# Performance work log

Hardware: AMD Instinct MI355X
Metric: run time of the kernel (lower is better)

The kernel has to match this reference:

```python
import jax, jax.numpy as jnp
import numpy as np

D_MODEL = 1024
N_HEADS = 16
D_HEAD = D_MODEL // N_HEADS
B = 2
Q_LEN = 1024
MEM_LEN = 1024
K_LEN = MEM_LEN + Q_LEN


def _split_heads(x, n_heads):
    b, t, d = x.shape
    return x.reshape(b, t, n_heads, d // n_heads).transpose(0, 2, 1, 3)


def _rel_shift(x):
    # x: [b, h, q, k] -> Transformer-XL relative shift
    b, h, q_len, k_len = x.shape
    x = jnp.pad(x, ((0, 0), (0, 0), (0, 0), (1, 0)))
    x = x.reshape(b, h, k_len + 1, q_len)
    x = x[:, :, 1:, :]
    return x.reshape(b, h, q_len, k_len)


def setup_inputs() -> dict:
    key = jax.random.key(0)
    ks = jax.random.split(key, 10)
    s = 1.0 / np.sqrt(D_MODEL)  # lecun_normal-ish scale for kernels
    return {
        "h": jax.random.normal(ks[0], (B, Q_LEN, D_MODEL), jnp.float32),
        "mem": jax.random.normal(ks[1], (B, MEM_LEN, D_MODEL), jnp.float32),
        "r": jax.random.normal(ks[2], (K_LEN, D_MODEL), jnp.float32),
        "Wq": jax.random.normal(ks[3], (D_MODEL, D_MODEL), jnp.float32) * s,
        "Wk": jax.random.normal(ks[4], (D_MODEL, D_MODEL), jnp.float32) * s,
        "Wv": jax.random.normal(ks[5], (D_MODEL, D_MODEL), jnp.float32) * s,
        "Wr": jax.random.normal(ks[6], (D_MODEL, D_MODEL), jnp.float32) * s,
        "Wo": jax.random.normal(ks[7], (D_MODEL, D_MODEL), jnp.float32) * s,
        "r_w_bias": jnp.zeros((N_HEADS, D_HEAD), jnp.float32),
        "r_r_bias": jnp.zeros((N_HEADS, D_HEAD), jnp.float32),
    }


def reference(h, mem, r, Wq, Wk, Wv, Wr, Wo, r_w_bias, r_r_bias):
    k_len = mem.shape[1] + h.shape[1]
    cat = jnp.concatenate([mem, h], axis=1)           # [b, k, d]
    q = _split_heads(h @ Wq, N_HEADS)                  # [b, h, q, dh]
    k = _split_heads(cat @ Wk, N_HEADS)                # [b, h, k, dh]
    v = _split_heads(cat @ Wv, N_HEADS)                # [b, h, k, dh]
    r_head = (r @ Wr).reshape(k_len, N_HEADS, D_HEAD).transpose(1, 0, 2)  # [h, k, dh]

    qw = q + r_w_bias[None, :, None, :]
    ac = jnp.einsum('bhqd,bhkd->bhqk', qw, k)          # content score
    qr = q + r_r_bias[None, :, None, :]
    bd = _rel_shift(jnp.einsum('bhqd,hkd->bhqk', qr, r_head))  # position score

    attn_score = (ac + bd) / jnp.sqrt(jnp.array(D_HEAD, jnp.float32))
    attn_prob = jax.nn.softmax(attn_score, axis=-1)
    attn_vec = jnp.einsum('bhqk,bhkd->bhqd', attn_prob, v)
    b, nh, t, dh = attn_vec.shape
    attn_vec = attn_vec.transpose(0, 2, 1, 3).reshape(b, t, nh * dh)
    return attn_vec @ Wo
```

## Files before the change

kernel.cpp:

```cpp
#include <hip/hip_runtime.h>

#define DM 1024
#define NH 16
#define DH 64
#define QL 1024
#define KL 2048

typedef short s16x8 __attribute__((ext_vector_type(8)));
typedef float f32x4 __attribute__((ext_vector_type(4)));

__device__ __forceinline__ unsigned short f2bf(float f) {
  unsigned int u = __builtin_bit_cast(unsigned int, f);
  u += 0x7fffu + ((u >> 16) & 1u);
  return (unsigned short)(u >> 16);
}
__device__ __forceinline__ float bf2f(unsigned short b) {
  unsigned int u = ((unsigned int)b) << 16;
  return __builtin_bit_cast(float, u);
}
__device__ __forceinline__ f32x4 mfma16(s16x8 a, s16x8 b, f32x4 c) {
  return __builtin_amdgcn_mfma_f32_16x16x32_bf16(a, b, c, 0, 0, 0);
}
__device__ __forceinline__ void gl2lds16(const void* g, void* l) {
  __builtin_amdgcn_global_load_lds(
      (const __attribute__((address_space(1))) unsigned int*)g,
      (__attribute__((address_space(3))) unsigned int*)l, 16, 0, 0);
}


__global__ __launch_bounds__(256) void prep_all(
    const float* __restrict__ h, const float* __restrict__ mem, const float* __restrict__ r,
    const float* __restrict__ Wq, const float* __restrict__ Wk, const float* __restrict__ Wv,
    const float* __restrict__ Wr, const float* __restrict__ Wo,
    unsigned short* __restrict__ catb, unsigned short* __restrict__ rb,
    unsigned short* __restrict__ wqt, unsigned short* __restrict__ wkvt,
    unsigned short* __restrict__ wrt,
    unsigned short* __restrict__ wohi, unsigned short* __restrict__ wolo)
{
  __shared__ unsigned short tH[64][72];
  __shared__ unsigned short tL[64][72];
  if (blockIdx.x < 6144) {
    int idx = blockIdx.x * 256 + threadIdx.x;
    if (idx < 1048576) {
      int e = idx * 4;
      int row = e >> 10, col = e & 1023;
      int b = row >> 11, t = row & 2047;
      const float* s = (t < 1024) ? &mem[((size_t)(b * 1024 + t)) * 1024 + col]
                                  : &h[((size_t)(b * 1024 + t - 1024)) * 1024 + col];
      float4 v = *(const float4*)s;
      *(ushort4*)&catb[e] = make_ushort4(f2bf(v.x), f2bf(v.y), f2bf(v.z), f2bf(v.w));
    } else {
      int e = (idx - 1048576) * 4;
      float4 v = *(const float4*)&r[e];
      *(ushort4*)&rb[e] = make_ushort4(f2bf(v.x), f2bf(v.y), f2bf(v.z), f2bf(v.w));
    }
    return;
  }
  int q = blockIdx.x - 6144;
  int job = q >> 8;
  int tb = q & 255;
  int sr0 = (tb >> 4) * 64, sc0 = (tb & 15) * 64;
  const float* src = (job == 0) ? Wq : (job == 1) ? Wk : (job == 2) ? Wv : (job == 3) ? Wr : Wo;
  int tid = threadIdx.x;
  int rr = tid >> 4, c4 = (tid & 15) * 4;
#pragma unroll
  for (int i = 0; i < 4; ++i) {
    int row = rr + i * 16;
    float4 v = *(const float4*)&src[(size_t)(sr0 + row) * 1024 + sc0 + c4];
    float vv[4] = {v.x, v.y, v.z, v.w};
#pragma unroll
    for (int j = 0; j < 4; ++j) {
      unsigned short hi = f2bf(vv[j]);
      tH[c4 + j][row] = hi;
      if (job == 4) tL[c4 + j][row] = f2bf(vv[j] - bf2f(hi));
    }
  }
  __syncthreads();
  unsigned short* dst = (job == 0) ? wqt : (job == 1) ? wkvt
                      : (job == 2) ? (wkvt + (size_t)1024 * 1024)
                      : (job == 3) ? wrt : wohi;
#pragma unroll
  for (int i = 0; i < 4; ++i) {
    int row = rr + i * 16;
    size_t o = (size_t)(sc0 + row) * 1024 + sr0 + c4;
    *(ushort4*)&dst[o] = make_ushort4(tH[row][c4], tH[row][c4 + 1], tH[row][c4 + 2], tH[row][c4 + 3]);
    if (job == 4)
      *(ushort4*)&wolo[o] = make_ushort4(tL[row][c4], tL[row][c4 + 1], tL[row][c4 + 2], tL[row][c4 + 3]);
  }
}

__global__ __launch_bounds__(256) void gemm_all(
    const unsigned short* __restrict__ catb, const unsigned short* __restrict__ rb,
    const unsigned short* __restrict__ wqt, const unsigned short* __restrict__ wkvt,
    const unsigned short* __restrict__ wrt,
    const float* __restrict__ rwb, const float* __restrict__ rrb,
    unsigned short* __restrict__ qwP, unsigned short* __restrict__ qrP,
    unsigned short* __restrict__ kP, unsigned short* __restrict__ vP,
    unsigned short* __restrict__ rP)
{
  __shared__ __align__(16) unsigned short As[2 * 128 * 32];
  __shared__ __align__(16) unsigned short Bs[2 * 128 * 32];
  int blk = blockIdx.x, tid = threadIdx.x;
  int job, mb, nb;
  const unsigned short *A, *Bt;
  if (blk < 128)      { job = 0; A = catb; Bt = wqt;  mb = blk >> 3; nb = blk & 7; }
  else if (blk < 640) { job = 1; A = catb; Bt = wkvt; int q = blk - 128; mb = q >> 4; nb = q & 15; }
  else                { job = 2; A = rb;   Bt = wrt;  int q = blk - 640; mb = q >> 3; nb = q & 7; }

  const int w = tid >> 6;
  const int r0 = tid >> 2;
  const int c0u = (tid & 3) * 8;
  int ga_r0 = mb * 128 + r0, ga_r1 = mb * 128 + 64 + r0;
  if (job == 0) {
    ga_r0 = ((ga_r0 >> 10) << 11) + 1024 + (ga_r0 & 1023);
    ga_r1 = ((ga_r1 >> 10) << 11) + 1024 + (ga_r1 & 1023);
  }
  const unsigned short* gA0 = A + (size_t)ga_r0 * 1024 + c0u;
  const unsigned short* gA1 = A + (size_t)ga_r1 * 1024 + c0u;
  const unsigned short* gB0 = Bt + (size_t)(nb * 128 + r0) * 1024 + c0u;
  const unsigned short* gB1 = Bt + (size_t)(nb * 128 + 64 + r0) * 1024 + c0u;
  char* lA0 = (char*)As + w * 1024;  char* lA1 = (char*)As + 4096 + w * 1024;
  char* lB0 = (char*)Bs + w * 1024;  char* lB1 = (char*)Bs + 4096 + w * 1024;

  const int lane = tid & 63;
  const int lc = lane & 15, quad = lane >> 4;
  const int wm = (w & 1) * 64, wn = (w >> 1) * 64;

  f32x4 acc[4][4];
#pragma unroll
  for (int mt = 0; mt < 4; ++mt)
#pragma unroll
    for (int nt = 0; nt < 4; ++nt) { acc[mt][nt][0] = 0.f; acc[mt][nt][1] = 0.f; acc[mt][nt][2] = 0.f; acc[mt][nt][3] = 0.f; }

  for (int k0 = 0; k0 < 1024; k0 += 64) {
    __syncthreads();
    gl2lds16(gA0 + k0, lA0);
    gl2lds16(gA1 + k0, lA1);
    gl2lds16(gB0 + k0, lB0);
    gl2lds16(gB1 + k0, lB1);
    gl2lds16(gA0 + k0 + 32, lA0 + 8192);
    gl2lds16(gA1 + k0 + 32, lA1 + 8192);
    gl2lds16(gB0 + k0 + 32, lB0 + 8192);
    gl2lds16(gB1 + k0 + 32, lB1 + 8192);
    __syncthreads();
#pragma unroll
    for (int s = 0; s < 2; ++s) {
      s16x8 af[4], bfr[4];
#pragma unroll
      for (int mt = 0; mt < 4; ++mt) af[mt] = *(const s16x8*)&As[s * 4096 + (wm + mt * 16 + lc) * 32 + quad * 8];
#pragma unroll
      for (int nt = 0; nt < 4; ++nt) bfr[nt] = *(const s16x8*)&Bs[s * 4096 + (wn + nt * 16 + lc) * 32 + quad * 8];
#pragma unroll
      for (int mt = 0; mt < 4; ++mt)
#pragma unroll
        for (int nt = 0; nt < 4; ++nt) acc[mt][nt] = mfma16(af[mt], bfr[nt], acc[mt][nt]);
    }
  }

#pragma unroll
  for (int mt = 0; mt < 4; ++mt) {
    int t4 = mb * 128 + wm + mt * 16 + quad * 4;
#pragma unroll
    for (int nt = 0; nt < 4; ++nt) {
      int n = nb * 128 + wn + nt * 16 + lc;
      if (job == 0) {
        int hh = n >> 6, dh = n & 63;
        int f = dh >> 5, qd = (dh >> 3) & 3, j = dh & 7;
        float bw = rwb[n], br = rrb[n];
        int bb = t4 >> 10, trow = t4 & 1023;
        size_t tbb = ((((size_t)(bb * NH + hh) * 64 + (trow >> 4)) * 2 + f) * 512) + qd * 128 + j;
        int l0 = trow & 15;
#pragma unroll
        for (int rr = 0; rr < 4; ++rr) {
          qwP[tbb + (l0 + rr) * 8] = f2bf(acc[mt][nt][rr] + bw);
          qrP[tbb + (l0 + rr) * 8] = f2bf(acc[mt][nt][rr] + br);
        }
      } else if (job == 1) {
        int bb = t4 >> 11, t = t4 & 2047;
        if (n < 1024) {
          int hh = n >> 6, dh = n & 63;
          int f = dh >> 5, qd = (dh >> 3) & 3, j = dh & 7;
          size_t tbb = ((((size_t)(bb * NH + hh) * 128 + (t >> 4)) * 2 + f) * 512) + qd * 128 + j;
          int l0 = t & 15;
#pragma unroll
          for (int rr = 0; rr < 4; ++rr)
            kP[tbb + (l0 + rr) * 8] = f2bf(acc[mt][nt][rr]);
        } else {
          int n2 = n - 1024, hh = n2 >> 6, dh = n2 & 63;
          int bhv = bb * NH + hh;
          int kt = t >> 5;
          int ntv = dh >> 4;
          int lanev = (((t >> 3) & 3) << 4) + (dh & 15);
          ushort4 pk = make_ushort4(f2bf(acc[mt][nt][0]), f2bf(acc[mt][nt][1]),
                                    f2bf(acc[mt][nt][2]), f2bf(acc[mt][nt][3]));
          *(ushort4*)&vP[(((size_t)bhv * 64 + kt) * 4 + ntv) * 512 + lanev * 8 + (t & 7)] = pk;
        }
      } else {
        int hh = n >> 6, dh = n & 63;
        int f = dh >> 5, qd = (dh >> 3) & 3, j = dh & 7;
        size_t tbb = (((size_t)hh * 128 + (t4 >> 4)) * 2 + f) * 512 + qd * 128 + j;
        int l0 = t4 & 15;
#pragma unroll
        for (int rr = 0; rr < 4; ++rr)
          rP[tbb + (l0 + rr) * 8] = f2bf(acc[mt][nt][rr]);
      }
    }
  }
}

#define BDSTR 2058
__global__ __launch_bounds__(512, 4) void attn(
    const unsigned short* __restrict__ qwP, const unsigned short* __restrict__ qrP,
    const unsigned short* __restrict__ kP, const unsigned short* __restrict__ vP,
    const unsigned short* __restrict__ rP,
    unsigned short* __restrict__ avhi, unsigned short* __restrict__ avlo)
{
  __shared__ __align__(16) unsigned short bdS[17 * BDSTR];
  __shared__ __align__(16) unsigned short pS[8 * 16 * 36];
  float* oS = (float*)bdS;
  float* lS = (float*)bdS + 8192;

  const int tid = threadIdx.x;
  const int w = tid >> 6, lane = tid & 63;
  const int lc = lane & 15, quad = lane >> 4;
  const int is = blockIdx.x & 63, h = (blockIdx.x >> 6) & 15, b = blockIdx.x >> 10;
  const int i0 = is * 16;
  const size_t bh = (size_t)b * NH + h;

  const unsigned short* qwP_p = qwP + bh * 65536;
  const unsigned short* qrP_p = qrP + bh * 65536;
  const unsigned short* kP_p  = kP + bh * 131072;
  const unsigned short* vP_p  = vP + bh * (size_t)KL * DH + lane * 8;
  const unsigned short* rP_p  = rP + (size_t)h * 131072;

  {
    const int cmax = 1006 - i0;
    s16x8 qa00 = *(const s16x8*)(qrP_p + is * 1024 + lane * 8);
    s16x8 qa01 = *(const s16x8*)(qrP_p + is * 1024 + 512 + lane * 8);
    int r1 = i0 + 16 + lc; if (r1 > 1023) r1 = 1023;
    int off1 = (r1 >> 4) * 1024 + (quad * 16 + (r1 & 15)) * 8;
    s16x8 qa10 = *(const s16x8*)(qrP_p + off1);
    s16x8 qa11 = *(const s16x8*)(qrP_p + off1 + 512);
    const int xt0 = w * 16;
    const unsigned short* rp = rP_p + xt0 * 1024 + lane * 8;
    s16x8 rf0 = *(const s16x8*)rp;
    s16x8 rf1 = *(const s16x8*)(rp + 512);
    for (int xt = xt0; xt < xt0 + 16; ++xt) {
      s16x8 cf0 = rf0, cf1 = rf1;
      if (xt + 1 < xt0 + 16) {
        const unsigned short* rpn = rP_p + (xt + 1) * 1024 + lane * 8;
        rf0 = *(const s16x8*)rpn;
        rf1 = *(const s16x8*)(rpn + 512);
      }
      f32x4 c0; c0[0] = 0.f; c0[1] = 0.f; c0[2] = 0.f; c0[3] = 0.f;
      c0 = mfma16(qa00, cf0, c0); c0 = mfma16(qa01, cf1, c0);
      int col = xt * 16 + lc;
#pragma unroll
      for (int rr = 0; rr < 4; ++rr) bdS[(quad * 4 + rr) * BDSTR + col] = f2bf(c0[rr]);
      if (xt * 16 <= cmax) {
        f32x4 c1; c1[0] = 0.f; c1[1] = 0.f; c1[2] = 0.f; c1[3] = 0.f;
        c1 = mfma16(qa10, cf0, c1); c1 = mfma16(qa11, cf1, c1);
        if (lane < 16) bdS[16 * BDSTR + col] = f2bf(c1[0]);
      }
    }
  }
  __syncthreads();

  s16x8 qwf0 = *(const s16x8*)(qwP_p + is * 1024 + lane * 8);
  s16x8 qwf1 = *(const s16x8*)(qwP_p + is * 1024 + 512 + lane * 8);

  f32x4 O[4];
#pragma unroll
  for (int nt = 0; nt < 4; ++nt) { O[nt][0] = 0.f; O[nt][1] = 0.f; O[nt][2] = 0.f; O[nt][3] = 0.f; }
  float lsum[4] = {0.f, 0.f, 0.f, 0.f};
  unsigned short* pw = pS + w * 16 * 36;
  int ebase[4];
#pragma unroll
  for (int rr = 0; rr < 4; ++rr) ebase[rr] = lc - (quad * 4 + rr) - i0;

  auto gatherBD = [&](int k0, float bd[2][4]) {
#pragma unroll
    for (int tt = 0; tt < 2; ++tt)
#pragma unroll
      for (int rr = 0; rr < 4; ++rr) {
        int row = quad * 4 + rr;
        int d = k0 + tt * 16 + ebase[rr];
        int am = row * BDSTR + (d + 1023);
        int aw = (row + 1) * BDSTR + (d - 1026);
        unsigned short vb = bdS[(d <= 1024) ? am : aw];
        bd[tt][rr] = (d == 1025) ? 0.0f : bf2f(vb);
      }
  };
  auto loadK4 = [&](int k0, s16x8& a0, s16x8& a1, s16x8& b0, s16x8& b1) {
    const unsigned short* kp = kP_p + (size_t)(k0 >> 4) * 1024 + lane * 8;
    a0 = *(const s16x8*)kp;
    a1 = *(const s16x8*)(kp + 512);
    b0 = *(const s16x8*)(kp + 1024);
    b1 = *(const s16x8*)(kp + 1536);
  };
  const float E2S = 0.18033688011112042f;
  const float E2B = -17.312340490667562f;
  auto qkExp = [&](const s16x8& a0, const s16x8& a1, const s16x8& b0, const s16x8& b1,
                   const float bd[2][4], float p[2][4]) {
    f32x4 c;
    c[0] = bd[0][0]; c[1] = bd[0][1]; c[2] = bd[0][2]; c[3] = bd[0][3];
    c = mfma16(qwf0, a0, c);
    c = mfma16(qwf1, a1, c);
#pragma unroll
    for (int rr = 0; rr < 4; ++rr) {
      p[0][rr] = __builtin_amdgcn_exp2f(fmaf(c[rr], E2S, E2B));
      lsum[rr] += p[0][rr];
    }
    f32x4 d;
    d[0] = bd[1][0]; d[1] = bd[1][1]; d[2] = bd[1][2]; d[3] = bd[1][3];
    d = mfma16(qwf0, b0, d);
    d = mfma16(qwf1, b1, d);
#pragma unroll
    for (int rr = 0; rr < 4; ++rr) {
      p[1][rr] = __builtin_amdgcn_exp2f(fmaf(d[rr], E2S, E2B));
      lsum[rr] += p[1][rr];
    }
  };
  auto storeP = [&](float p[2][4]) {
#pragma unroll
    for (int rr = 0; rr < 4; ++rr) {
      int row = quad * 4 + rr;
      pw[row * 36 + lc]      = f2bf(p[0][rr]);
      pw[row * 36 + 16 + lc] = f2bf(p[1][rr]);
    }
  };
  auto loadV = [&](int k0, s16x8 vf[4]) {
    const unsigned short* base = vP_p + (size_t)(k0 >> 5) * 2048;
#pragma unroll
    for (int nt = 0; nt < 4; ++nt)
      vf[nt] = *(const s16x8*)(base + nt * 512);
  };

  s16x8 ka0, ka1, kb0, kb1;
  s16x8 vfPrev[4];
  loadK4(w * 256, ka0, ka1, kb0, kb1);
  loadV(w * 256, vfPrev);
  {
    float bd[2][4], p[2][4];
    gatherBD(w * 256, bd);
    s16x8 na0, na1, nb0, nb1;
    loadK4(w * 256 + 32, na0, na1, nb0, nb1);
    qkExp(ka0, ka1, kb0, kb1, bd, p);
    storeP(p);
    ka0 = na0; ka1 = na1; kb0 = nb0; kb1 = nb1;
  }
#pragma unroll 1
  for (int it = 1; it < 8; ++it) {
    const int k0 = w * 256 + it * 32;
    __builtin_amdgcn_s_waitcnt(0xC07F);
    s16x8 pf = *(const s16x8*)(pw + lc * 36 + quad * 8);
    float bd[2][4], p[2][4];
    gatherBD(k0, bd);
    s16x8 na0, na1, nb0, nb1;
    const int kn = k0 + ((it < 7) ? 32 : 0);
    loadK4(kn, na0, na1, nb0, nb1);
#pragma unroll
    for (int nt = 0; nt < 4; ++nt) O[nt] = mfma16(pf, vfPrev[nt], O[nt]);
    loadV(k0, vfPrev);
    qkExp(ka0, ka1, kb0, kb1, bd, p);
    storeP(p);
    ka0 = na0; ka1 = na1; kb0 = nb0; kb1 = nb1;
  }
  {
    __builtin_amdgcn_s_waitcnt(0xC07F);
    s16x8 pf = *(const s16x8*)(pw + lc * 36 + quad * 8);
#pragma unroll
    for (int nt = 0; nt < 4; ++nt) O[nt] = mfma16(pf, vfPrev[nt], O[nt]);
  }

#pragma unroll
  for (int msk = 1; msk <= 8; msk <<= 1)
#pragma unroll
    for (int rr = 0; rr < 4; ++rr) lsum[rr] += __shfl_xor(lsum[rr], msk);

  __syncthreads();
#pragma unroll
  for (int nt = 0; nt < 4; ++nt)
#pragma unroll
    for (int rr = 0; rr < 4; ++rr)
      oS[(w * 16 + quad * 4 + rr) * 64 + nt * 16 + lc] = O[nt][rr];
  if (lc == 0) {
#pragma unroll
    for (int rr = 0; rr < 4; ++rr) lS[w * 16 + quad * 4 + rr] = lsum[rr];
  }
  __syncthreads();

  if (tid < 256) {
    int r = tid >> 4, c0 = (tid & 15) * 4;
    float L = 0.f, a0 = 0.f, a1 = 0.f, a2 = 0.f, a3 = 0.f;
#pragma unroll
    for (int wv = 0; wv < 8; ++wv) {
      L += lS[wv * 16 + r];
      const float* op = oS + (wv * 16 + r) * 64 + c0;
      a0 += op[0]; a1 += op[1]; a2 += op[2]; a3 += op[3];
    }
    float inv = 1.0f / L;
    float v[4] = {a0 * inv, a1 * inv, a2 * inv, a3 * inv};
    unsigned short hi[4], lo[4];
#pragma unroll
    for (int j = 0; j < 4; ++j) {
      hi[j] = f2bf(v[j]);
      lo[j] = f2bf(v[j] - bf2f(hi[j]));
    }
    size_t oidx = ((size_t)(b * QL + i0 + r)) * DM + h * DH + c0;
    *(ushort4*)&avhi[oidx] = make_ushort4(hi[0], hi[1], hi[2], hi[3]);
    *(ushort4*)&avlo[oidx] = make_ushort4(lo[0], lo[1], lo[2], lo[3]);
  }
}

__global__ __launch_bounds__(256) void gemm_final(
    const unsigned short* __restrict__ avhi, const unsigned short* __restrict__ avlo,
    const unsigned short* __restrict__ wohi, const unsigned short* __restrict__ wolo,
    float* __restrict__ out)
{
  __shared__ __align__(16) unsigned short S[4][2][64 * 32];
  int blk = blockIdx.x, tid = threadIdx.x;
  int mb = blk >> 4, nb = blk & 15;

  const int w = tid >> 6, lane = tid & 63;
  const int srow = w * 16 + (lane >> 2);
  const int scu = (lane & 3) * 8;
  const size_t arow = (size_t)(mb * 64 + srow) * 1024 + scu;
  const size_t brow = (size_t)(nb * 64 + srow) * 1024 + scu;
  char* l0 = (char*)&S[0][0][0] + w * 1024;
  char* l1 = (char*)&S[1][0][0] + w * 1024;
  char* l2 = (char*)&S[2][0][0] + w * 1024;
  char* l3 = (char*)&S[3][0][0] + w * 1024;

  const int lc = lane & 15, quad = lane >> 4;
  const int wm = (w & 1) * 32, wn = (w >> 1) * 32;

  f32x4 acc[2][2];
#pragma unroll
  for (int mt = 0; mt < 2; ++mt)
#pragma unroll
    for (int nt = 0; nt < 2; ++nt) { acc[mt][nt][0] = 0.f; acc[mt][nt][1] = 0.f; acc[mt][nt][2] = 0.f; acc[mt][nt][3] = 0.f; }

  for (int k0 = 0; k0 < 1024; k0 += 64) {
    __syncthreads();
    gl2lds16(avhi + arow + k0, l0);
    gl2lds16(avhi + arow + k0 + 32, l0 + 4096);
    gl2lds16(avlo + arow + k0, l1);
    gl2lds16(avlo + arow + k0 + 32, l1 + 4096);
    gl2lds16(wohi + brow + k0, l2);
    gl2lds16(wohi + brow + k0 + 32, l2 + 4096);
    gl2lds16(wolo + brow + k0, l3);
    gl2lds16(wolo + brow + k0 + 32, l3 + 4096);
    __syncthreads();
#pragma unroll
    for (int s = 0; s < 2; ++s) {
      s16x8 ah[2], al[2], bh[2], bl[2];
#pragma unroll
      for (int mt = 0; mt < 2; ++mt) {
        int off = (wm + mt * 16 + lc) * 32 + quad * 8;
        ah[mt] = *(const s16x8*)&S[0][s][off];
        al[mt] = *(const s16x8*)&S[1][s][off];
      }
#pragma unroll
      for (int nt = 0; nt < 2; ++nt) {
        int off = (wn + nt * 16 + lc) * 32 + quad * 8;
        bh[nt] = *(const s16x8*)&S[2][s][off];
        bl[nt] = *(const s16x8*)&S[3][s][off];
      }
#pragma unroll
      for (int mt = 0; mt < 2; ++mt)
#pragma unroll
        for (int nt = 0; nt < 2; ++nt) {
          acc[mt][nt] = mfma16(ah[mt], bh[nt], acc[mt][nt]);
          acc[mt][nt] = mfma16(ah[mt], bl[nt], acc[mt][nt]);
          acc[mt][nt] = mfma16(al[mt], bh[nt], acc[mt][nt]);
        }
    }
  }

#pragma unroll
  for (int mt = 0; mt < 2; ++mt)
#pragma unroll
    for (int nt = 0; nt < 2; ++nt) {
      int n = nb * 64 + wn + nt * 16 + lc;
#pragma unroll
      for (int rr = 0; rr < 4; ++rr) {
        int m = mb * 64 + wm + mt * 16 + quad * 4 + rr;
        out[(size_t)m * 1024 + n] = acc[mt][nt][rr];
      }
    }
}

extern "C" void kernel_launch(void* const* d_in, const int* in_sizes, int n_in,
                              void* d_out, int out_size, void* d_ws, size_t ws_size,
                              hipStream_t stream) {
  (void)in_sizes; (void)n_in; (void)out_size; (void)ws_size;
  const float* h   = (const float*)d_in[0];
  const float* mem = (const float*)d_in[1];
  const float* r   = (const float*)d_in[2];
  const float* Wq  = (const float*)d_in[3];
  const float* Wk  = (const float*)d_in[4];
  const float* Wv  = (const float*)d_in[5];
  const float* Wr  = (const float*)d_in[6];
  const float* Wo  = (const float*)d_in[7];
  const float* rwb = (const float*)d_in[8];
  const float* rrb = (const float*)d_in[9];
  float* out = (float*)d_out;

  char* ws = (char*)d_ws;
  unsigned short* catb = (unsigned short*)(ws + 0);
  unsigned short* rb   = (unsigned short*)(ws + 8388608);
  unsigned short* wqt  = (unsigned short*)(ws + 12582912);
  unsigned short* wkvt = (unsigned short*)(ws + 14680064);
  unsigned short* wrt  = (unsigned short*)(ws + 18874368);
  unsigned short* wohi = (unsigned short*)(ws + 20971520);
  unsigned short* wolo = (unsigned short*)(ws + 23068672);
  unsigned short* qwP  = (unsigned short*)(ws + 25165824);
  unsigned short* qrP  = (unsigned short*)(ws + 29360128);
  unsigned short* kPb  = (unsigned short*)(ws + 33554432);
  unsigned short* vPb  = (unsigned short*)(ws + 41943040);
  unsigned short* rPb  = (unsigned short*)(ws + 50331648);
  unsigned short* avhi = (unsigned short*)(ws + 54525952);
  unsigned short* avlo = (unsigned short*)(ws + 58720256);

  prep_all<<<7424, 256, 0, stream>>>(h, mem, r, Wq, Wk, Wv, Wr, Wo,
                                     catb, rb, wqt, wkvt, wrt, wohi, wolo);
  gemm_all<<<768, 256, 0, stream>>>(catb, rb, wqt, wkvt, wrt, rwb, rrb,
                                    qwP, qrP, kPb, vPb, rPb);
  attn<<<2048, 512, 0, stream>>>(qwP, qrP, kPb, vPb, rPb, avhi, avlo);
  gemm_final<<<512, 256, 0, stream>>>(avhi, avlo, wohi, wolo, out);
}
```

Measured before the change: 260.3 us.

## Double-buffer GEMM k-tiles and pipeline attention BD gather and P·V

Both projection GEMMs (gemm_all and gemm_final) now use two LDS buffers with 32-wide k-steps. The next k-tile's global-to-LDS load is issued before the current tile's MFMAs, so memory latency overlaps compute. The attention inner loop now prefetches the next tile's rel-shift BD gather alongside the next K loads, and moves the P·V MFMA after the QK exponent work. It also drops the explicit s_waitcnt and instead reads the P fragment right after storing it. These changes trade extra registers (nbd, a second pf) for overlap, at some risk of lower occupancy or of relying on the compiler's LDS ordering.

```diff
diff --git a/kernel.cpp b/kernel.cpp
--- a/kernel.cpp
+++ b/kernel.cpp
@@ -98,8 +98,8 @@
     unsigned short* __restrict__ kP, unsigned short* __restrict__ vP,
     unsigned short* __restrict__ rP)
 {
-  __shared__ __align__(16) unsigned short As[2 * 128 * 32];
-  __shared__ __align__(16) unsigned short Bs[2 * 128 * 32];
+  __shared__ __align__(16) unsigned short As[2][128 * 32];
+  __shared__ __align__(16) unsigned short Bs[2][128 * 32];
   int blk = blockIdx.x, tid = threadIdx.x;
   int job, mb, nb;
   const unsigned short *A, *Bt;
@@ -119,42 +119,39 @@
   const unsigned short* gA1 = A + (size_t)ga_r1 * 1024 + c0u;
   const unsigned short* gB0 = Bt + (size_t)(nb * 128 + r0) * 1024 + c0u;
   const unsigned short* gB1 = Bt + (size_t)(nb * 128 + 64 + r0) * 1024 + c0u;
-  char* lA0 = (char*)As + w * 1024;  char* lA1 = (char*)As + 4096 + w * 1024;
-  char* lB0 = (char*)Bs + w * 1024;  char* lB1 = (char*)Bs + 4096 + w * 1024;
 
   const int lane = tid & 63;
   const int lc = lane & 15, quad = lane >> 4;
   const int wm = (w & 1) * 64, wn = (w >> 1) * 64;
 
+  auto stage = [&](int k0, int bi) {
+    gl2lds16(gA0 + k0, (char*)As[bi] + w * 1024);
+    gl2lds16(gA1 + k0, (char*)As[bi] + 4096 + w * 1024);
+    gl2lds16(gB0 + k0, (char*)Bs[bi] + w * 1024);
+    gl2lds16(gB1 + k0, (char*)Bs[bi] + 4096 + w * 1024);
+  };
+
   f32x4 acc[4][4];
 #pragma unroll
   for (int mt = 0; mt < 4; ++mt)
 #pragma unroll
     for (int nt = 0; nt < 4; ++nt) { acc[mt][nt][0] = 0.f; acc[mt][nt][1] = 0.f; acc[mt][nt][2] = 0.f; acc[mt][nt][3] = 0.f; }
 
-  for (int k0 = 0; k0 < 1024; k0 += 64) {
+  stage(0, 0);
+  __syncthreads();
+  for (int k0 = 0; k0 < 1024; k0 += 32) {
+    int cur = (k0 >> 5) & 1;
+    if (k0 + 32 < 1024) stage(k0 + 32, cur ^ 1);
+    s16x8 af[4], bfr[4];
+#pragma unroll
+    for (int mt = 0; mt < 4; ++mt) af[mt] = *(const s16x8*)&As[cur][(wm + mt * 16 + lc) * 32 + quad * 8];
+#pragma unroll
+    for (int nt = 0; nt < 4; ++nt) bfr[nt] = *(const s16x8*)&Bs[cur][(wn + nt * 16 + lc) * 32 + quad * 8];
+#pragma unroll
+    for (int mt = 0; mt < 4; ++mt)
+#pragma unroll
+      for (int nt = 0; nt < 4; ++nt) acc[mt][nt] = mfma16(af[mt], bfr[nt], acc[mt][nt]);
     __syncthreads();
-    gl2lds16(gA0 + k0, lA0);
-    gl2lds16(gA1 + k0, lA1);
-    gl2lds16(gB0 + k0, lB0);
-    gl2lds16(gB1 + k0, lB1);
-    gl2lds16(gA0 + k0 + 32, lA0 + 8192);
-    gl2lds16(gA1 + k0 + 32, lA1 + 8192);
-    gl2lds16(gB0 + k0 + 32, lB0 + 8192);
-    gl2lds16(gB1 + k0 + 32, lB1 + 8192);
-    __syncthreads();
-#pragma unroll
-    for (int s = 0; s < 2; ++s) {
-      s16x8 af[4], bfr[4];
-#pragma unroll
-      for (int mt = 0; mt < 4; ++mt) af[mt] = *(const s16x8*)&As[s * 4096 + (wm + mt * 16 + lc) * 32 + quad * 8];
-#pragma unroll
-      for (int nt = 0; nt < 4; ++nt) bfr[nt] = *(const s16x8*)&Bs[s * 4096 + (wn + nt * 16 + lc) * 32 + quad * 8];
-#pragma unroll
-      for (int mt = 0; mt < 4; ++mt)
-#pragma unroll
-        for (int nt = 0; nt < 4; ++nt) acc[mt][nt] = mfma16(af[mt], bfr[nt], acc[mt][nt]);
-    }
   }
 
 #pragma unroll
@@ -336,41 +333,52 @@
       vf[nt] = *(const s16x8*)(base + nt * 512);
   };
 
+  const int base = w * 256;
   s16x8 ka0, ka1, kb0, kb1;
-  s16x8 vfPrev[4];
-  loadK4(w * 256, ka0, ka1, kb0, kb1);
-  loadV(w * 256, vfPrev);
+  s16x8 vf[4];
+  s16x8 pf;
+  float bd[2][4], nbd[2][4];
+
+  gatherBD(base, bd);
+  loadK4(base, ka0, ka1, kb0, kb1);
+  loadV(base, vf);
   {
-    float bd[2][4], p[2][4];
-    gatherBD(w * 256, bd);
+    float p[2][4];
+    gatherBD(base + 32, nbd);
     s16x8 na0, na1, nb0, nb1;
-    loadK4(w * 256 + 32, na0, na1, nb0, nb1);
+    loadK4(base + 32, na0, na1, nb0, nb1);
     qkExp(ka0, ka1, kb0, kb1, bd, p);
     storeP(p);
+    pf = *(const s16x8*)(pw + lc * 36 + quad * 8);
     ka0 = na0; ka1 = na1; kb0 = nb0; kb1 = nb1;
+#pragma unroll
+    for (int tt = 0; tt < 2; ++tt)
+#pragma unroll
+      for (int rr = 0; rr < 4; ++rr) bd[tt][rr] = nbd[tt][rr];
   }
 #pragma unroll 1
-  for (int it = 1; it < 8; ++it) {
-    const int k0 = w * 256 + it * 32;
-    __builtin_amdgcn_s_waitcnt(0xC07F);
-    s16x8 pf = *(const s16x8*)(pw + lc * 36 + quad * 8);
-    float bd[2][4], p[2][4];
-    gatherBD(k0, bd);
+  for (int s = 1; s < 8; ++s) {
+    const int k0 = base + s * 32;
+    const int kn = base + ((s < 7) ? (s + 1) * 32 : s * 32);
+    float p[2][4];
+    gatherBD(kn, nbd);
     s16x8 na0, na1, nb0, nb1;
-    const int kn = k0 + ((it < 7) ? 32 : 0);
     loadK4(kn, na0, na1, nb0, nb1);
-#pragma unroll
-    for (int nt = 0; nt < 4; ++nt) O[nt] = mfma16(pf, vfPrev[nt], O[nt]);
-    loadV(k0, vfPrev);
     qkExp(ka0, ka1, kb0, kb1, bd, p);
+#pragma unroll
+    for (int nt = 0; nt < 4; ++nt) O[nt] = mfma16(pf, vf[nt], O[nt]);
+    loadV(k0, vf);
     storeP(p);
+    pf = *(const s16x8*)(pw + lc * 36 + quad * 8);
     ka0 = na0; ka1 = na1; kb0 = nb0; kb1 = nb1;
+#pragma unroll
+    for (int tt = 0; tt < 2; ++tt)
+#pragma unroll
+      for (int rr = 0; rr < 4; ++rr) bd[tt][rr] = nbd[tt][rr];
   }
   {
-    __builtin_amdgcn_s_waitcnt(0xC07F);
-    s16x8 pf = *(const s16x8*)(pw + lc * 36 + quad * 8);
-#pragma unroll
-    for (int nt = 0; nt < 4; ++nt) O[nt] = mfma16(pf, vfPrev[nt], O[nt]);
+#pragma unroll
+    for (int nt = 0; nt < 4; ++nt) O[nt] = mfma16(pf, vf[nt], O[nt]);
   }
 
 #pragma unroll
@@ -418,7 +426,7 @@
     const unsigned short* __restrict__ wohi, const unsigned short* __restrict__ wolo,
     float* __restrict__ out)
 {
-  __shared__ __align__(16) unsigned short S[4][2][64 * 32];
+  __shared__ __align__(16) unsigned short S[2][4][64 * 32];
   int blk = blockIdx.x, tid = threadIdx.x;
   int mb = blk >> 4, nb = blk & 15;
 
@@ -427,55 +435,50 @@
   const int scu = (lane & 3) * 8;
   const size_t arow = (size_t)(mb * 64 + srow) * 1024 + scu;
   const size_t brow = (size_t)(nb * 64 + srow) * 1024 + scu;
-  char* l0 = (char*)&S[0][0][0] + w * 1024;
-  char* l1 = (char*)&S[1][0][0] + w * 1024;
-  char* l2 = (char*)&S[2][0][0] + w * 1024;
-  char* l3 = (char*)&S[3][0][0] + w * 1024;
 
   const int lc = lane & 15, quad = lane >> 4;
   const int wm = (w & 1) * 32, wn = (w >> 1) * 32;
 
+  auto stage = [&](int k0, int bi) {
+    gl2lds16(avhi + arow + k0, (char*)S[bi][0] + w * 1024);
+    gl2lds16(avlo + arow + k0, (char*)S[bi][1] + w * 1024);
+    gl2lds16(wohi + brow + k0, (char*)S[bi][2] + w * 1024);
+    gl2lds16(wolo + brow + k0, (char*)S[bi][3] + w * 1024);
+  };
+
   f32x4 acc[2][2];
 #pragma unroll
   for (int mt = 0; mt < 2; ++mt)
 #pragma unroll
     for (int nt = 0; nt < 2; ++nt) { acc[mt][nt][0] = 0.f; acc[mt][nt][1] = 0.f; acc[mt][nt][2] = 0.f; acc[mt][nt][3] = 0.f; }
 
-  for (int k0 = 0; k0 < 1024; k0 += 64) {
+  stage(0, 0);
+  __syncthreads();
+  for (int k0 = 0; k0 < 1024; k0 += 32) {
+    int cur = (k0 >> 5) & 1;
+    if (k0 + 32 < 1024) stage(k0 + 32, cur ^ 1);
+    s16x8 ah[2], al[2], bh[2], bl[2];
+#pragma unroll
+    for (int mt = 0; mt < 2; ++mt) {
+      int off = (wm + mt * 16 + lc) * 32 + quad * 8;
+      ah[mt] = *(const s16x8*)&S[cur][0][off];
+      al[mt] = *(const s16x8*)&S[cur][1][off];
+    }
+#pragma unroll
+    for (int nt = 0; nt < 2; ++nt) {
+      int off = (wn + nt * 16 + lc) * 32 + quad * 8;
+      bh[nt] = *(const s16x8*)&S[cur][2][off];
+      bl[nt] = *(const s16x8*)&S[cur][3][off];
+    }
+#pragma unroll
+    for (int mt = 0; mt < 2; ++mt)
+#pragma unroll
+      for (int nt = 0; nt < 2; ++nt) {
+        acc[mt][nt] = mfma16(ah[mt], bh[nt], acc[mt][nt]);
+        acc[mt][nt] = mfma16(ah[mt], bl[nt], acc[mt][nt]);
+        acc[mt][nt] = mfma16(al[mt], bh[nt], acc[mt][nt]);
+      }
     __syncthreads();
-    gl2lds16(avhi + arow + k0, l0);
-    gl2lds16(avhi + arow + k0 + 32, l0 + 4096);
-    gl2lds16(avlo + arow + k0, l1);
-    gl2lds16(avlo + arow + k0 + 32, l1 + 4096);
-    gl2lds16(wohi + brow + k0, l2);
-    gl2lds16(wohi + brow + k0 + 32, l2 + 4096);
-    gl2lds16(wolo + brow + k0, l3);
-    gl2lds16(wolo + brow + k0 + 32, l3 + 4096);
-    __syncthreads();
-#pragma unroll
-    for (int s = 0; s < 2; ++s) {
-      s16x8 ah[2], al[2], bh[2], bl[2];
-#pragma unroll
-      for (int mt = 0; mt < 2; ++mt) {
-        int off = (wm + mt * 16 + lc) * 32 + quad * 8;
-        ah[mt] = *(const s16x8*)&S[0][s][off];
-        al[mt] = *(const s16x8*)&S[1][s][off];
-      }
-#pragma unroll
-      for (int nt = 0; nt < 2; ++nt) {
-        int off = (wn + nt * 16 + lc) * 32 + quad * 8;
-        bh[nt] = *(const s16x8*)&S[2][s][off];
-        bl[nt] = *(const s16x8*)&S[3][s][off];
-      }
-#pragma unroll
-      for (int mt = 0; mt < 2; ++mt)
-#pragma unroll
-        for (int nt = 0; nt < 2; ++nt) {
-          acc[mt][nt] = mfma16(ah[mt], bh[nt], acc[mt][nt]);
-          acc[mt][nt] = mfma16(ah[mt], bl[nt], acc[mt][nt]);
-          acc[mt][nt] = mfma16(al[mt], bh[nt], acc[mt][nt]);
-        }
-    }
   }
 
 #pragma unroll
```

Result: faster. 239.9 us (-7.8%).
